# Performance work log

Measured on AMD Instinct MI355X. Metric: run time of the kernel, lower is better.

Reference implementation:

```python
import math
import jax, jax.numpy as jnp
import numpy as np
from jax import lax

N, C, H, W = 8, 256, 56, 56
S41, S42, S14 = 1, -1, 1  # fixed values for random roll shifts in original __init__


def setup_inputs() -> dict:
    key = jax.random.key(0)
    ks = jax.random.split(key, 9)
    c8 = C // 8
    x = jax.random.normal(ks[0], (N, C, H, W), jnp.float32)
    p2 = jax.random.normal(ks[1], (1, C, H, W), jnp.float32) * 0.02
    w6 = jax.random.normal(ks[2], (c8, C), jnp.float32) * (1.0 / math.sqrt(C))
    w7 = jax.random.normal(ks[3], (C, 9 * C), jnp.float32) * (1.0 / math.sqrt(9 * C))
    p9 = jax.random.normal(ks[4], (1, c8, H, W), jnp.float32) * 0.02
    b11 = math.sqrt(3.0 / c8)
    p11 = jax.random.uniform(ks[5], (c8, 1), jnp.float32, -b11, b11)
    w12 = jax.random.normal(ks[6], (C, 1, 3, 1), jnp.float32) * (1.0 / math.sqrt(3.0))
    w15 = jax.random.normal(ks[7], (C, C), jnp.float32) * (1.0 / math.sqrt(C))
    b16 = math.sqrt(3.0 / C)
    p16 = jax.random.uniform(ks[8], (C, H * W), jnp.float32, -b16, b16)
    return dict(x=x, p2=p2, w6=w6, w7=w7, p9=p9, p11=p11, w12=w12, w15=w15, p16=p16)


def _unfold33_d3(x):
    # F.unfold(x, (3,3), dilation=(3,3), padding=(3,3)) -> (n, c, 3, 3, h, w)
    xp = jnp.pad(x, ((0, 0), (0, 0), (3, 3), (3, 3)))
    rows = [jnp.stack([xp[:, :, 3 * i:3 * i + H, 3 * j:3 * j + W] for j in range(3)], axis=2)
            for i in range(3)]
    return jnp.stack(rows, axis=2)


def _forward(x, p2, w6, w7, p9, p11, w12, w15, p16):
    n = x.shape[0]
    s_hw = 1.0 / math.sqrt(H * W)
    s_c = 1.0 / math.sqrt(C)
    t1 = _unfold33_d3(x)                                    # n,c,3,3,h,w
    t2 = p2 * x
    t3 = t2 * t2
    t4 = jnp.roll(jnp.roll(t3, S41, axis=2), S42, axis=3)
    t5 = jax.nn.softmax(t4, axis=2)                          # softmax over h
    t6 = jnp.einsum('nchw,oc->nohw', t3, w6)                 # 1x1 conv c -> c//8
    t7 = jnp.einsum('nkhw,ok->nohw', t1.reshape(n, 9 * C, H, W), w7)  # 1x1 conv 9c -> c
    t8 = jnp.einsum('ncs,nds->ncd', t5.reshape(n, C, H * W), t3.reshape(n, C, H * W)) * s_hw
    t9 = p9 * t6
    t10 = jnp.maximum(t5, t7)
    t11 = jnp.einsum('nbhw,be->nehw', t9, p11)[:, 0]         # (n,h,w)
    # depthwise conv, kernel (3,1), dilation (2,1), padding (2,0)
    t12 = lax.conv_general_dilated(t10, w12, window_strides=(1, 1),
                                   padding=((2, 2), (0, 0)), rhs_dilation=(2, 1),
                                   feature_group_count=C,
                                   dimension_numbers=('NCHW', 'OIHW', 'NCHW'))
    t13 = t11[:, None] - t12                                 # (n,c,h,w)
    t14 = jnp.roll(x, S14, axis=2)
    t15 = jnp.einsum('nchw,oc->nohw', t14, w15)              # 1x1 conv c -> c
    t16 = jnp.einsum('nbc,bd->ndc', t8, p16)                 # (n, hw, c)
    t17 = t3 - t15
    t18 = t7 * t17
    t19 = jnp.einsum('ncs,nsd->ncd', t17.reshape(n, C, H * W), t16) * s_hw  # (n,c,c)
    t20 = (jnp.einsum('ndc,nds->ncs', t19, t13.reshape(n, C, H * W)) * s_c).reshape(n, C, H, W)
    return t20 + t18


def reference(x, p2, w6, w7, p9, p11, w12, w15, p16):
    return _forward(x, p2, w6, w7, p9, p11, w12, w15, p16)
```

## Files before the change

kernel.cpp:

```cpp
#include <hip/hip_runtime.h>

#define Nn 8
#define Cc 256
#define C8 32
#define Hh 56
#define Ww 56
#define HW 3136
#define CHW (Cc * HW)
#define K9C 2304
#define S_HW (1.0f / 56.0f)
#define S_C  0.0625f
#define XPLANE 3844
#define XPAD_ELEMS (Nn * XPLANE * Cc)

typedef float f4 __attribute__((ext_vector_type(4)));
typedef unsigned short ushort;
typedef __attribute__((ext_vector_type(4))) unsigned short u16x4;
typedef __attribute__((ext_vector_type(8))) unsigned short u16x8;
typedef __attribute__((ext_vector_type(8))) short short8;
typedef __attribute__((ext_vector_type(4))) float floatx4;

__device__ __forceinline__ ushort f2bf(float f) {
    union { float f; unsigned u; } v; v.f = f;
    unsigned r = v.u + 0x7FFF + ((v.u >> 16) & 1);
    return (ushort)(r >> 16);
}
__device__ __forceinline__ float bf2f(ushort u) {
    union { unsigned u; float f; } v; v.u = ((unsigned)u) << 16;
    return v.f;
}

__global__ __launch_bounds__(256) void k_t3(const float* __restrict__ x,
                                            const float* __restrict__ p2,
                                            float* __restrict__ t3,
                                            ushort* __restrict__ t3b) {
    int g = blockIdx.x * 256 + threadIdx.x;
    int idx = g * 4;
    int pidx = idx % CHW;
    f4 xv = *(const f4*)(x + idx);
    f4 pv = *(const f4*)(p2 + pidx);
    f4 t = xv * pv;
    f4 q = t * t;
    *(f4*)(t3 + idx) = q;
    u16x4 qb = { f2bf(q[0]), f2bf(q[1]), f2bf(q[2]), f2bf(q[3]) };
    *(u16x4*)(t3b + idx) = qb;
}

__global__ __launch_bounds__(256) void k_xT(const float* __restrict__ x,
                                            ushort* __restrict__ xpT) {
    __shared__ ushort Ts[112][40];
    int tid = threadIdx.x;
    int n = blockIdx.z;
    int c0 = blockIdx.y * 32;
    int s0 = blockIdx.x * 112;
    const float* xn = x + (size_t)n * CHW;
#pragma unroll
    for (int e = 0; e < 4; e++) {
        int lin = tid + e * 256;
        int sq = lin & 31;
        int c_l = lin >> 5;
        if (sq < 28) {
            f4 v = *(const f4*)(xn + (size_t)(c0 + c_l) * HW + s0 + sq * 4);
#pragma unroll
            for (int k = 0; k < 4; k++) Ts[sq * 4 + k][c_l] = f2bf(v[k]);
        }
    }
    __syncthreads();
    ushort* dstn = xpT + (size_t)n * (XPLANE * Cc);
#pragma unroll
    for (int e = 0; e < 2; e++) {
        int lin = tid + e * 256;
        int r = lin >> 2, ch = lin & 3;
        if (r < 112) {
            u16x8 v = *(const u16x8*)(&Ts[r][ch * 8]);
            int s_g = s0 + r;
            int h = s_g / 56;
            int wc = s_g - h * 56;
            size_t drow = (size_t)((h + 3) * 62 + wc + 3);
            *(u16x8*)(dstn + drow * Cc + c0 + ch * 8) = v;
        }
    }
}

__global__ __launch_bounds__(256) void k_w7p(const float* __restrict__ w7,
                                             ushort* __restrict__ w7p) {
    int g = blockIdx.x * 256 + threadIdx.x;
    int ij = g >> 16;
    int rem = g & 65535;
    int o = rem >> 8;
    int c = rem & 255;
    w7p[g] = f2bf(w7[(size_t)o * K9C + c * 9 + ij]);
}

__global__ __launch_bounds__(256) void k_cvt(const float* __restrict__ src,
                                             ushort* __restrict__ dst) {
    int g = blockIdx.x * 256 + threadIdx.x;
    dst[g] = f2bf(src[g]);
}

__global__ __launch_bounds__(256) void k_softmax(const float* __restrict__ t3,
                                                 ushort* __restrict__ t5b) {
    __shared__ float ld[HW];
    __shared__ float mx[Ww], rs[Ww];
    int tid = threadIdx.x;
    const float* src = t3 + (size_t)blockIdx.x * HW;
    for (int i = tid; i < HW; i += 256) ld[i] = src[i];
    __syncthreads();
    if (tid < Ww) {
        float m = -1e30f;
        for (int h = 0; h < Hh; h++) m = fmaxf(m, ld[h * Ww + tid]);
        float s = 0.f;
        for (int h = 0; h < Hh; h++) s += __expf(ld[h * Ww + tid] - m);
        mx[tid] = m;
        rs[tid] = 1.0f / s;
    }
    __syncthreads();
    ushort* dst = t5b + (size_t)blockIdx.x * HW;
    for (int i = tid; i < HW; i += 256) {
        int h = i / Ww, w = i - h * Ww;
        int wp = (w + 1 == Ww) ? 0 : w + 1;
        int hp = (h == 0) ? Hh - 1 : h - 1;
        dst[i] = f2bf(__expf(ld[hp * Ww + wp] - mx[wp]) * rs[wp]);
    }
}

__global__ __launch_bounds__(256, 3) void k_gemm_t7_mfma(
        const ushort* __restrict__ xpT,
        const ushort* __restrict__ w7p,
        float* __restrict__ t7) {
    __shared__ __align__(16) ushort Bs[620][40];
    int tid = threadIdx.x;
    int lane = tid & 63;
    int ln15 = lane & 15, quad = lane >> 4;
    int wave = tid >> 6;
    int wo = (wave >> 1) * 32;
    int wsx = (wave & 1) * 112;
    int n = blockIdx.z;
    int hb = blockIdx.y;
    int o0 = blockIdx.x * 64;
    const ushort* xT = xpT + (size_t)n * (XPLANE * Cc);
    size_t stageBase = (size_t)(hb * 248) * Cc;

    int sp0[7];
#pragma unroll
    for (int f = 0; f < 7; f++) {
        int s_l = wsx + f * 16 + ln15;
        int orow = s_l / 56;
        int wv = s_l - orow * 56;
        sp0[f] = orow * 62 + wv;
    }

    floatx4 acc[2][7] = {};

    for (int ct = 0; ct < Cc; ct += 32) {
        __syncthreads();
#pragma unroll
        for (int e = 0; e < 10; e++) {
            int lin = tid + e * 256;
            if (lin < 2480) {
                int sp = lin >> 2, ch = lin & 3;
                u16x8 v = *(const u16x8*)(xT + stageBase + (size_t)sp * Cc + ct + ch * 8);
                *(u16x8*)(&Bs[sp][ch * 8]) = v;
            }
        }
        __syncthreads();
        const ushort* wp = w7p + ct + quad * 8;
#pragma unroll
        for (int ij = 0; ij < 9; ij++) {
            int dsp = (ij / 3) * 186 + (ij % 3) * 3;
            short8 a0 = *(const short8*)(wp + (size_t)(ij * 256 + o0 + wo + ln15) * Cc);
            short8 a1 = *(const short8*)(wp + (size_t)(ij * 256 + o0 + wo + 16 + ln15) * Cc);
#pragma unroll
            for (int f = 0; f < 7; f++) {
                short8 b = *(const short8*)(&Bs[sp0[f] + dsp][quad * 8]);
                acc[0][f] = __builtin_amdgcn_mfma_f32_16x16x32_bf16(a0, b, acc[0][f], 0, 0, 0);
                acc[1][f] = __builtin_amdgcn_mfma_f32_16x16x32_bf16(a1, b, acc[1][f], 0, 0, 0);
            }
        }
    }

    float* t7n = t7 + (size_t)n * CHW;
    int sBase = hb * 224 + wsx;
#pragma unroll
    for (int m = 0; m < 2; m++) {
        int obase = o0 + wo + m * 16 + quad * 4;
#pragma unroll
        for (int f = 0; f < 7; f++) {
            int s = sBase + f * 16 + ln15;
#pragma unroll
            for (int r = 0; r < 4; r++)
                t7n[(size_t)(obase + r) * HW + s] = acc[m][f][r];
        }
    }
}

__global__ __launch_bounds__(256) void k_gemm_t15_mfma(const float* __restrict__ x,
                                                       const ushort* __restrict__ w15b,
                                                       const float* __restrict__ t3,
                                                       ushort* __restrict__ t17b) {
    __shared__ __align__(16) ushort As[128][40];
    __shared__ __align__(16) ushort Bs[128][40];
    int tid = threadIdx.x;
    int lane = tid & 63;
    int ln15 = lane & 15;
    int quad = lane >> 4;
    int wave = tid >> 6;
    int wm64 = (wave >> 1) * 64;
    int wn64 = (wave & 1) * 64;
    int n = blockIdx.z;
    int s0 = blockIdx.x * 128;
    int o0 = blockIdx.y * 128;
    const float* xn = x + (size_t)n * CHW;

    floatx4 acc[4][4] = {};

    for (int kt = 0; kt < Cc; kt += 32) {
#pragma unroll
        for (int e = 0; e < 2; e++) {
            int lin = tid + e * 256;
            int m = lin >> 2, kq = (lin & 3) * 8;
            *(u16x8*)(&As[m][kq]) =
                *(const u16x8*)(w15b + (size_t)(o0 + m) * Cc + kt + kq);
        }
#pragma unroll
        for (int e = 0; e < 4; e++) {
            int lin = tid + e * 256;
            int c_l = lin >> 5;
            int s4 = (lin & 31) * 4;
            int s = s0 + s4;
            int sc = s < HW ? s : HW - 4;
            int h = sc / Ww;
            int s_src = (h == 0) ? sc + 3080 : sc - 56;
            f4 v = *(const f4*)(xn + (size_t)(kt + c_l) * HW + s_src);
            Bs[s4 + 0][c_l] = f2bf(v[0]);
            Bs[s4 + 1][c_l] = f2bf(v[1]);
            Bs[s4 + 2][c_l] = f2bf(v[2]);
            Bs[s4 + 3][c_l] = f2bf(v[3]);
        }
        __syncthreads();

        short8 af[4], bf[4];
#pragma unroll
        for (int a = 0; a < 4; a++)
            af[a] = *(const short8*)(&As[wm64 + a * 16 + ln15][quad * 8]);
#pragma unroll
        for (int b = 0; b < 4; b++)
            bf[b] = *(const short8*)(&Bs[wn64 + b * 16 + ln15][quad * 8]);
#pragma unroll
        for (int a = 0; a < 4; a++)
#pragma unroll
            for (int b = 0; b < 4; b++)
                acc[a][b] = __builtin_amdgcn_mfma_f32_16x16x32_bf16(
                    af[a], bf[b], acc[a][b], 0, 0, 0);
        __syncthreads();
    }

    const float* t3n = t3 + (size_t)n * CHW;
    ushort* t17n = t17b + (size_t)n * CHW;
#pragma unroll
    for (int a = 0; a < 4; a++) {
        int obase = o0 + wm64 + a * 16 + quad * 4;
#pragma unroll
        for (int b = 0; b < 4; b++) {
            int s = s0 + wn64 + b * 16 + ln15;
            if (s < HW) {
#pragma unroll
                for (int r = 0; r < 4; r++) {
                    size_t idx = (size_t)(obase + r) * HW + s;
                    t17n[idx] = f2bf(t3n[idx] - acc[a][b][r]);
                }
            }
        }
    }
}

__global__ __launch_bounds__(256) void k_gemm_abt_mfma(const ushort* __restrict__ A,
                                                       const ushort* __restrict__ B,
                                                       long Bn,
                                                       float* __restrict__ outp,
                                                       float scale) {
    __shared__ __align__(16) ushort As[128][40];
    __shared__ __align__(16) ushort Bs[128][40];
    int tid = threadIdx.x;
    int lane = tid & 63;
    int ln15 = lane & 15;
    int quad = lane >> 4;
    int wave = tid >> 6;
    int wm64 = (wave >> 1) * 64;
    int wn64 = (wave & 1) * 64;
    int z = blockIdx.z;
    int n = z / 7, ks = z - n * 7;
    int d0 = blockIdx.x * 128;
    int c0 = blockIdx.y * 128;
    const ushort* An = A + (size_t)n * CHW;
    const ushort* Bb = B + (size_t)n * Bn;

    floatx4 acc[4][4] = {};
    int kbeg = ks * 448;

    for (int kt = kbeg; kt < kbeg + 448; kt += 32) {
#pragma unroll
        for (int e = 0; e < 2; e++) {
            int lin = tid + e * 256;
            int m = lin >> 2, kq = (lin & 3) * 8;
            *(u16x8*)(&As[m][kq]) =
                *(const u16x8*)(An + (size_t)(c0 + m) * HW + kt + kq);
            *(u16x8*)(&Bs[m][kq]) =
                *(const u16x8*)(Bb + (size_t)(d0 + m) * HW + kt + kq);
        }
        __syncthreads();

        short8 af[4], bf[4];
#pragma unroll
        for (int a = 0; a < 4; a++)
            af[a] = *(const short8*)(&As[wm64 + a * 16 + ln15][quad * 8]);
#pragma unroll
        for (int b = 0; b < 4; b++)
            bf[b] = *(const short8*)(&Bs[wn64 + b * 16 + ln15][quad * 8]);
#pragma unroll
        for (int a = 0; a < 4; a++)
#pragma unroll
            for (int b = 0; b < 4; b++)
                acc[a][b] = __builtin_amdgcn_mfma_f32_16x16x32_bf16(
                    af[a], bf[b], acc[a][b], 0, 0, 0);
        __syncthreads();
    }

    float* on = outp + (size_t)n * (Cc * Cc);
#pragma unroll
    for (int a = 0; a < 4; a++) {
        int cbase = c0 + wm64 + a * 16 + quad * 4;
#pragma unroll
        for (int b = 0; b < 4; b++) {
            int d = d0 + wn64 + b * 16 + ln15;
#pragma unroll
            for (int r = 0; r < 4; r++)
                atomicAdd(&on[(size_t)(cbase + r) * Cc + d], acc[a][b][r] * scale);
        }
    }
}

__global__ __launch_bounds__(256) void k_gemm_t19(const float* __restrict__ u,
                                                  const float* __restrict__ t8,
                                                  ushort* __restrict__ t19Tb) {
    __shared__ float As[64][20];
    __shared__ float Bs[16][68];
    int tid = threadIdx.x;
    int tx = tid & 15, ty = tid >> 4;
    int n = blockIdx.z;
    int d0 = blockIdx.x * 64;
    int c0 = blockIdx.y * 64;
    const float* un = u + (size_t)n * Cc * Cc;
    const float* t8n = t8 + (size_t)n * Cc * Cc;
    f4 acc[4] = {};
    for (int kt = 0; kt < Cc; kt += 16) {
        int lin = tid * 4;
        {
            int r = lin >> 4, kq = lin & 15;
            *(f4*)(&As[r][kq]) = *(const f4*)(un + (size_t)(c0 + r) * Cc + kt + kq);
        }
        {
            int kk = lin >> 6, col = lin & 63;
            *(f4*)(&Bs[kk][col]) = *(const f4*)(t8n + (size_t)(kt + kk) * Cc + d0 + col);
        }
        __syncthreads();
#pragma unroll
        for (int kk = 0; kk < 16; kk += 4) {
            f4 av[4], bv[4];
#pragma unroll
            for (int a = 0; a < 4; a++) av[a] = *(const f4*)(&As[ty * 4 + a][kk]);
#pragma unroll
            for (int q = 0; q < 4; q++) bv[q] = *(const f4*)(&Bs[kk + q][tx * 4]);
#pragma unroll
            for (int a = 0; a < 4; a++)
#pragma unroll
                for (int q = 0; q < 4; q++) acc[a] += av[a][q] * bv[q];
        }
        __syncthreads();
    }
    ushort* on = t19Tb + (size_t)n * Cc * Cc;
#pragma unroll
    for (int a = 0; a < 4; a++) {
        int c = c0 + ty * 4 + a;
#pragma unroll
        for (int j = 0; j < 4; j++)
            on[(size_t)(d0 + tx * 4 + j) * Cc + c] = f2bf(acc[a][j] * S_HW);
    }
}

__global__ __launch_bounds__(256) void k_t11(const float* __restrict__ t3,
                                             const float* __restrict__ w6,
                                             const float* __restrict__ p9,
                                             const float* __restrict__ p11,
                                             float* __restrict__ t11) {
    __shared__ float smem[8704];
    float* w6s = smem;
    float* part = smem;
    float* part2 = smem + 8448;
    int tid = threadIdx.x;
    for (int i = tid; i < C8 * Cc; i += 256) w6s[i] = w6[i];
    __syncthreads();
    int n = blockIdx.y;
    int sl = tid & 63;
    int cg = tid >> 6;
    int s = blockIdx.x * 64 + sl;
    const float* t3n = t3 + (size_t)n * CHW + s;
    float acc[C8] = {};
    for (int c = cg * 64; c < cg * 64 + 64; c += 4) {
        float v0 = t3n[(c + 0) * HW];
        float v1 = t3n[(c + 1) * HW];
        float v2 = t3n[(c + 2) * HW];
        float v3 = t3n[(c + 3) * HW];
#pragma unroll
        for (int b = 0; b < C8; b++) {
            f4 wv = *(const f4*)(&w6s[b * Cc + c]);
            acc[b] += wv[0] * v0 + wv[1] * v1 + wv[2] * v2 + wv[3] * v3;
        }
    }
    __syncthreads();
#pragma unroll
    for (int b = 0; b < C8; b++) part[(cg * 64 + sl) * 33 + b] = acc[b];
    __syncthreads();
    float r = 0.f;
#pragma unroll
    for (int j = 0; j < 8; j++) {
        int b = cg * 8 + j;
        float sum = part[(0 * 64 + sl) * 33 + b] + part[(1 * 64 + sl) * 33 + b] +
                    part[(2 * 64 + sl) * 33 + b] + part[(3 * 64 + sl) * 33 + b];
        r += p11[b] * p9[b * HW + s] * sum;
    }
    part2[cg * 64 + sl] = r;
    __syncthreads();
    if (tid < 64)
        t11[(size_t)n * HW + s] = part2[sl] + part2[64 + sl] + part2[128 + sl] + part2[192 + sl];
}

__global__ __launch_bounds__(256) void k_t13(const ushort* __restrict__ t5b,
                                             const float* __restrict__ t7,
                                             const float* __restrict__ t11,
                                             const float* __restrict__ w12,
                                             ushort* __restrict__ t13b) {
    int g = blockIdx.x * 256 + threadIdx.x;
    int s = g % HW;
    int nc = g / HW;
    int c = nc % Cc;
    int n = nc / Cc;
    int h = s / Ww, w = s - h * Ww;
    float sum = 0.f;
#pragma unroll
    for (int kh = 0; kh < 3; kh++) {
        int hh = h - 2 + 2 * kh;
        if ((unsigned)hh < (unsigned)Hh) {
            size_t idx = (size_t)nc * HW + hh * Ww + w;
            float t10 = fmaxf(bf2f(t5b[idx]), t7[idx]);
            sum += w12[c * 3 + kh] * t10;
        }
    }
    t13b[g] = f2bf(t11[(size_t)n * HW + s] - sum);
}

__global__ __launch_bounds__(256) void k_gemm_out_mfma(const ushort* __restrict__ t19Tb,
                                                       const ushort* __restrict__ t13b,
                                                       const float* __restrict__ t7,
                                                       const ushort* __restrict__ t17b,
                                                       float* __restrict__ outp) {
    __shared__ __align__(16) ushort As[128][40];
    __shared__ __align__(16) ushort Bs[128][40];
    int tid = threadIdx.x;
    int lane = tid & 63;
    int ln15 = lane & 15;
    int quad = lane >> 4;
    int wave = tid >> 6;
    int wm64 = (wave >> 1) * 64;
    int wn64 = (wave & 1) * 64;
    int n = blockIdx.z;
    int s0 = blockIdx.x * 128;
    int c0 = blockIdx.y * 128;
    const ushort* An = t19Tb + (size_t)n * Cc * Cc;
    const ushort* t13n = t13b + (size_t)n * CHW;

    floatx4 acc[4][4] = {};

    for (int kt = 0; kt < Cc; kt += 32) {
#pragma unroll
        for (int e = 0; e < 2; e++) {
            int lin = tid + e * 256;
            int m = lin >> 2, kq = (lin & 3) * 8;
            *(u16x8*)(&As[m][kq]) =
                *(const u16x8*)(An + (size_t)(c0 + m) * Cc + kt + kq);
        }
#pragma unroll
        for (int e = 0; e < 2; e++) {
            int lin = tid + e * 256;
            int d_l = lin >> 4;
            int s8 = (lin & 15) * 8;
            int s = s0 + s8;
            int sc = s <= HW - 8 ? s : HW - 8;
            u16x8 v = *(const u16x8*)(t13n + (size_t)(kt + d_l) * HW + sc);
#pragma unroll
            for (int j = 0; j < 8; j++) Bs[s8 + j][d_l] = v[j];
        }
        __syncthreads();

        short8 af[4], bf[4];
#pragma unroll
        for (int a = 0; a < 4; a++)
            af[a] = *(const short8*)(&As[wm64 + a * 16 + ln15][quad * 8]);
#pragma unroll
        for (int b = 0; b < 4; b++)
            bf[b] = *(const short8*)(&Bs[wn64 + b * 16 + ln15][quad * 8]);
#pragma unroll
        for (int a = 0; a < 4; a++)
#pragma unroll
            for (int b = 0; b < 4; b++)
                acc[a][b] = __builtin_amdgcn_mfma_f32_16x16x32_bf16(
                    af[a], bf[b], acc[a][b], 0, 0, 0);
        __syncthreads();
    }

    const float* t7n = t7 + (size_t)n * CHW;
    const ushort* t17n = t17b + (size_t)n * CHW;
    float* on = outp + (size_t)n * CHW;
#pragma unroll
    for (int a = 0; a < 4; a++) {
        int cbase = c0 + wm64 + a * 16 + quad * 4;
#pragma unroll
        for (int b = 0; b < 4; b++) {
            int s = s0 + wn64 + b * 16 + ln15;
            if (s < HW) {
#pragma unroll
                for (int r = 0; r < 4; r++) {
                    size_t idx = (size_t)(cbase + r) * HW + s;
                    on[idx] = acc[a][b][r] * S_C + t7n[idx] * bf2f(t17n[idx]);
                }
            }
        }
    }
}

extern "C" void kernel_launch(void* const* d_in, const int* in_sizes, int n_in,
                              void* d_out, int out_size, void* d_ws, size_t ws_size,
                              hipStream_t stream) {
    const float* x   = (const float*)d_in[0];
    const float* p2  = (const float*)d_in[1];
    const float* w6  = (const float*)d_in[2];
    const float* w7  = (const float*)d_in[3];
    const float* p9  = (const float*)d_in[4];
    const float* p11 = (const float*)d_in[5];
    const float* w12 = (const float*)d_in[6];
    const float* w15 = (const float*)d_in[7];
    const float* p16 = (const float*)d_in[8];
    float* ws = (float*)d_ws;

    float* t3  = ws;
    float* t7  = ws + 6422528;
    float* t8  = ws + 12845056;
    float* uu  = ws + 13369344;
    float* t11 = ws + 13893632;
    ushort* ub  = (ushort*)(ws + 13919232);
    ushort* t5b   = ub;
    ushort* t3b   = ub + 6422528;
    ushort* t17b  = ub + 12845056;
    ushort* t13b  = ub + 19267584;
    ushort* xpT   = ub + 25690112;
    ushort* w7p   = ub + 33562624;
    ushort* w15b  = ub + 34152448;
    ushort* p16b  = ub + 34217984;
    ushort* t19Tb = ub + 35020800;
    float* outp = (float*)d_out;

    hipMemsetAsync(xpT, 0, (size_t)XPAD_ELEMS * 2, stream);
    k_t3<<<dim3(6272), dim3(256), 0, stream>>>(x, p2, t3, t3b);
    k_xT<<<dim3(28, 8, Nn), dim3(256), 0, stream>>>(x, xpT);
    k_w7p<<<dim3(2304), dim3(256), 0, stream>>>(w7, w7p);
    k_cvt<<<dim3(256),  dim3(256), 0, stream>>>(w15, w15b);
    k_cvt<<<dim3(3136), dim3(256), 0, stream>>>(p16, p16b);
    k_softmax<<<dim3(Nn * Cc), dim3(256), 0, stream>>>(t3, t5b);
    hipMemsetAsync(t8, 0, (size_t)Nn * Cc * Cc * 4, stream);
    hipMemsetAsync(uu, 0, (size_t)Nn * Cc * Cc * 4, stream);
    k_gemm_t7_mfma<<<dim3(4, 14, Nn), dim3(256), 0, stream>>>(xpT, w7p, t7);
    k_gemm_t15_mfma<<<dim3(25, 2, Nn), dim3(256), 0, stream>>>(x, w15b, t3, t17b);
    k_gemm_abt_mfma<<<dim3(2, 2, Nn * 7), dim3(256), 0, stream>>>(t5b, t3b, (long)CHW, t8, S_HW);
    k_t11<<<dim3(49, 8), dim3(256), 0, stream>>>(t3, w6, p9, p11, t11);
    k_gemm_abt_mfma<<<dim3(2, 2, Nn * 7), dim3(256), 0, stream>>>(t17b, p16b, 0L, uu, 1.0f);
    k_gemm_t19<<<dim3(4, 4, Nn), dim3(256), 0, stream>>>(uu, t8, t19Tb);
    k_t13<<<dim3(25088), dim3(256), 0, stream>>>(t5b, t7, t11, w12, t13b);
    k_gemm_out_mfma<<<dim3(25, 2, Nn), dim3(256), 0, stream>>>(t19Tb, t13b, t7, t17b, outp);
}
```

Baseline: 361.6 us.

## Fuse t3 with softmax, store intermediates in bf16, merge abt GEMMs, prefetch t7 stage

Merges the t3 elementwise kernel with the softmax so t3 is produced in shared memory and never written in fp32. t7 is stored as bf16, and t15 reads the pre-transposed padded bf16 x buffer instead of transposing fp32 x itself. The two split-K ABᵀ GEMMs become one launch, the t7 GEMM prefetches its next stage into registers, and t13 is vectorised to four elements per thread. The aim is less HBM traffic and fewer launches, at the cost of extra bf16 rounding on t3 and t7 in later stages and higher register pressure in the t7 GEMM.

```diff
diff --git a/kernel.cpp b/kernel.cpp
--- a/kernel.cpp
+++ b/kernel.cpp
@@ -30,20 +30,44 @@
     return v.f;
 }
 
-__global__ __launch_bounds__(256) void k_t3(const float* __restrict__ x,
-                                            const float* __restrict__ p2,
-                                            float* __restrict__ t3,
-                                            ushort* __restrict__ t3b) {
-    int g = blockIdx.x * 256 + threadIdx.x;
-    int idx = g * 4;
-    int pidx = idx % CHW;
-    f4 xv = *(const f4*)(x + idx);
-    f4 pv = *(const f4*)(p2 + pidx);
-    f4 t = xv * pv;
-    f4 q = t * t;
-    *(f4*)(t3 + idx) = q;
-    u16x4 qb = { f2bf(q[0]), f2bf(q[1]), f2bf(q[2]), f2bf(q[3]) };
-    *(u16x4*)(t3b + idx) = qb;
+__global__ __launch_bounds__(256) void k_t3sm(const float* __restrict__ x,
+                                              const float* __restrict__ p2,
+                                              ushort* __restrict__ t3b,
+                                              ushort* __restrict__ t5b) {
+    __shared__ float ld[HW];
+    __shared__ float mx[Ww], rs[Ww];
+    int tid = threadIdx.x;
+    int nc = blockIdx.x;
+    int c = nc & 255;
+    const float* xn = x + (size_t)nc * HW;
+    const float* pp = p2 + (size_t)c * HW;
+    ushort* t3n = t3b + (size_t)nc * HW;
+    for (int i = tid; i < 784; i += 256) {
+        f4 xv = *(const f4*)(xn + i * 4);
+        f4 pv = *(const f4*)(pp + i * 4);
+        f4 t = xv * pv;
+        f4 q = t * t;
+        *(f4*)(&ld[i * 4]) = q;
+        u16x4 qb = { f2bf(q[0]), f2bf(q[1]), f2bf(q[2]), f2bf(q[3]) };
+        *(u16x4*)(t3n + i * 4) = qb;
+    }
+    __syncthreads();
+    if (tid < Ww) {
+        float m = -1e30f;
+        for (int h = 0; h < Hh; h++) m = fmaxf(m, ld[h * Ww + tid]);
+        float s = 0.f;
+        for (int h = 0; h < Hh; h++) s += __expf(ld[h * Ww + tid] - m);
+        mx[tid] = m;
+        rs[tid] = 1.0f / s;
+    }
+    __syncthreads();
+    ushort* dst = t5b + (size_t)nc * HW;
+    for (int i = tid; i < HW; i += 256) {
+        int h = i / Ww, w = i - h * Ww;
+        int wp = (w + 1 == Ww) ? 0 : w + 1;
+        int hp = (h == 0) ? Hh - 1 : h - 1;
+        dst[i] = f2bf(__expf(ld[hp * Ww + wp] - mx[wp]) * rs[wp]);
+    }
 }
 
 __global__ __launch_bounds__(256) void k_xT(const float* __restrict__ x,
@@ -98,36 +122,10 @@
     dst[g] = f2bf(src[g]);
 }
 
-__global__ __launch_bounds__(256) void k_softmax(const float* __restrict__ t3,
-                                                 ushort* __restrict__ t5b) {
-    __shared__ float ld[HW];
-    __shared__ float mx[Ww], rs[Ww];
-    int tid = threadIdx.x;
-    const float* src = t3 + (size_t)blockIdx.x * HW;
-    for (int i = tid; i < HW; i += 256) ld[i] = src[i];
-    __syncthreads();
-    if (tid < Ww) {
-        float m = -1e30f;
-        for (int h = 0; h < Hh; h++) m = fmaxf(m, ld[h * Ww + tid]);
-        float s = 0.f;
-        for (int h = 0; h < Hh; h++) s += __expf(ld[h * Ww + tid] - m);
-        mx[tid] = m;
-        rs[tid] = 1.0f / s;
-    }
-    __syncthreads();
-    ushort* dst = t5b + (size_t)blockIdx.x * HW;
-    for (int i = tid; i < HW; i += 256) {
-        int h = i / Ww, w = i - h * Ww;
-        int wp = (w + 1 == Ww) ? 0 : w + 1;
-        int hp = (h == 0) ? Hh - 1 : h - 1;
-        dst[i] = f2bf(__expf(ld[hp * Ww + wp] - mx[wp]) * rs[wp]);
-    }
-}
-
 __global__ __launch_bounds__(256, 3) void k_gemm_t7_mfma(
         const ushort* __restrict__ xpT,
         const ushort* __restrict__ w7p,
-        float* __restrict__ t7) {
+        ushort* __restrict__ t7b) {
     __shared__ __align__(16) ushort Bs[620][40];
     int tid = threadIdx.x;
     int lane = tid & 63;
@@ -138,8 +136,7 @@
     int n = blockIdx.z;
     int hb = blockIdx.y;
     int o0 = blockIdx.x * 64;
-    const ushort* xT = xpT + (size_t)n * (XPLANE * Cc);
-    size_t stageBase = (size_t)(hb * 248) * Cc;
+    const ushort* stagePtr = xpT + (size_t)n * (XPLANE * Cc) + (size_t)(hb * 248) * Cc;
 
     int sp0[7];
 #pragma unroll
@@ -151,19 +148,31 @@
     }
 
     floatx4 acc[2][7] = {};
+    u16x8 pre[10];
+#pragma unroll
+    for (int e = 0; e < 10; e++) {
+        int lin = tid + e * 256;
+        if (lin < 2480)
+            pre[e] = *(const u16x8*)(stagePtr + (size_t)(lin >> 2) * Cc + (lin & 3) * 8);
+    }
 
     for (int ct = 0; ct < Cc; ct += 32) {
-        __syncthreads();
 #pragma unroll
         for (int e = 0; e < 10; e++) {
             int lin = tid + e * 256;
-            if (lin < 2480) {
-                int sp = lin >> 2, ch = lin & 3;
-                u16x8 v = *(const u16x8*)(xT + stageBase + (size_t)sp * Cc + ct + ch * 8);
-                *(u16x8*)(&Bs[sp][ch * 8]) = v;
+            if (lin < 2480)
+                *(u16x8*)(&Bs[lin >> 2][(lin & 3) * 8]) = pre[e];
+        }
+        __syncthreads();
+        if (ct + 32 < Cc) {
+#pragma unroll
+            for (int e = 0; e < 10; e++) {
+                int lin = tid + e * 256;
+                if (lin < 2480)
+                    pre[e] = *(const u16x8*)(stagePtr + (size_t)(lin >> 2) * Cc +
+                                             ct + 32 + (lin & 3) * 8);
             }
         }
-        __syncthreads();
         const ushort* wp = w7p + ct + quad * 8;
 #pragma unroll
         for (int ij = 0; ij < 9; ij++) {
@@ -177,9 +186,10 @@
                 acc[1][f] = __builtin_amdgcn_mfma_f32_16x16x32_bf16(a1, b, acc[1][f], 0, 0, 0);
             }
         }
-    }
-
-    float* t7n = t7 + (size_t)n * CHW;
+        __syncthreads();
+    }
+
+    ushort* t7n = t7b + (size_t)n * CHW;
     int sBase = hb * 224 + wsx;
 #pragma unroll
     for (int m = 0; m < 2; m++) {
@@ -189,14 +199,14 @@
             int s = sBase + f * 16 + ln15;
 #pragma unroll
             for (int r = 0; r < 4; r++)
-                t7n[(size_t)(obase + r) * HW + s] = acc[m][f][r];
-        }
-    }
-}
-
-__global__ __launch_bounds__(256) void k_gemm_t15_mfma(const float* __restrict__ x,
+                t7n[(size_t)(obase + r) * HW + s] = f2bf(acc[m][f][r]);
+        }
+    }
+}
+
+__global__ __launch_bounds__(256) void k_gemm_t15_mfma(const ushort* __restrict__ xpT,
                                                        const ushort* __restrict__ w15b,
-                                                       const float* __restrict__ t3,
+                                                       const ushort* __restrict__ t3b,
                                                        ushort* __restrict__ t17b) {
     __shared__ __align__(16) ushort As[128][40];
     __shared__ __align__(16) ushort Bs[128][40];
@@ -210,7 +220,19 @@
     int n = blockIdx.z;
     int s0 = blockIdx.x * 128;
     int o0 = blockIdx.y * 128;
-    const float* xn = x + (size_t)n * CHW;
+    const ushort* xT = xpT + (size_t)n * (XPLANE * Cc);
+
+    int sp_src[2];
+#pragma unroll
+    for (int e = 0; e < 2; e++) {
+        int s_l = (tid + e * 256) >> 2;
+        int s = s0 + s_l;
+        int sc = s < HW ? s : HW - 1;
+        int h = sc / Ww, w = sc - h * Ww;
+        int hp = (h == 0) ? 58 : h + 2;
+        sp_src[e] = hp * 62 + w + 3;
+    }
+    int chq = (tid & 3) * 8;
 
     floatx4 acc[4][4] = {};
 
@@ -223,19 +245,10 @@
                 *(const u16x8*)(w15b + (size_t)(o0 + m) * Cc + kt + kq);
         }
 #pragma unroll
-        for (int e = 0; e < 4; e++) {
-            int lin = tid + e * 256;
-            int c_l = lin >> 5;
-            int s4 = (lin & 31) * 4;
-            int s = s0 + s4;
-            int sc = s < HW ? s : HW - 4;
-            int h = sc / Ww;
-            int s_src = (h == 0) ? sc + 3080 : sc - 56;
-            f4 v = *(const f4*)(xn + (size_t)(kt + c_l) * HW + s_src);
-            Bs[s4 + 0][c_l] = f2bf(v[0]);
-            Bs[s4 + 1][c_l] = f2bf(v[1]);
-            Bs[s4 + 2][c_l] = f2bf(v[2]);
-            Bs[s4 + 3][c_l] = f2bf(v[3]);
+        for (int e = 0; e < 2; e++) {
+            int s_l = (tid + e * 256) >> 2;
+            *(u16x8*)(&Bs[s_l][chq]) =
+                *(const u16x8*)(xT + (size_t)sp_src[e] * Cc + kt + chq);
         }
         __syncthreads();
 
@@ -255,7 +268,7 @@
         __syncthreads();
     }
 
-    const float* t3n = t3 + (size_t)n * CHW;
+    const ushort* t3n = t3b + (size_t)n * CHW;
     ushort* t17n = t17b + (size_t)n * CHW;
 #pragma unroll
     for (int a = 0; a < 4; a++) {
@@ -267,18 +280,19 @@
 #pragma unroll
                 for (int r = 0; r < 4; r++) {
                     size_t idx = (size_t)(obase + r) * HW + s;
-                    t17n[idx] = f2bf(t3n[idx] - acc[a][b][r]);
+                    t17n[idx] = f2bf(bf2f(t3n[idx]) - acc[a][b][r]);
                 }
             }
         }
     }
 }
 
-__global__ __launch_bounds__(256) void k_gemm_abt_mfma(const ushort* __restrict__ A,
-                                                       const ushort* __restrict__ B,
-                                                       long Bn,
-                                                       float* __restrict__ outp,
-                                                       float scale) {
+__global__ __launch_bounds__(256) void k_abt2(const ushort* __restrict__ t5b,
+                                              const ushort* __restrict__ t3b,
+                                              const ushort* __restrict__ t17b,
+                                              const ushort* __restrict__ p16b,
+                                              float* __restrict__ t8,
+                                              float* __restrict__ uu) {
     __shared__ __align__(16) ushort As[128][40];
     __shared__ __align__(16) ushort Bs[128][40];
     int tid = threadIdx.x;
@@ -288,12 +302,15 @@
     int wave = tid >> 6;
     int wm64 = (wave >> 1) * 64;
     int wn64 = (wave & 1) * 64;
+    int sel = blockIdx.y >> 1;
+    int c0 = (blockIdx.y & 1) * 128;
+    int d0 = blockIdx.x * 128;
     int z = blockIdx.z;
     int n = z / 7, ks = z - n * 7;
-    int d0 = blockIdx.x * 128;
-    int c0 = blockIdx.y * 128;
-    const ushort* An = A + (size_t)n * CHW;
-    const ushort* Bb = B + (size_t)n * Bn;
+    const ushort* An = (sel ? t17b : t5b) + (size_t)n * CHW;
+    const ushort* Bb = sel ? p16b : (t3b + (size_t)n * CHW);
+    float* outp = (sel ? uu : t8) + (size_t)n * (Cc * Cc);
+    float scale = sel ? 1.0f : S_HW;
 
     floatx4 acc[4][4] = {};
     int kbeg = ks * 448;
@@ -326,7 +343,6 @@
         __syncthreads();
     }
 
-    float* on = outp + (size_t)n * (Cc * Cc);
 #pragma unroll
     for (int a = 0; a < 4; a++) {
         int cbase = c0 + wm64 + a * 16 + quad * 4;
@@ -335,7 +351,7 @@
             int d = d0 + wn64 + b * 16 + ln15;
 #pragma unroll
             for (int r = 0; r < 4; r++)
-                atomicAdd(&on[(size_t)(cbase + r) * Cc + d], acc[a][b][r] * scale);
+                atomicAdd(&outp[(size_t)(cbase + r) * Cc + d], acc[a][b][r] * scale);
         }
     }
 }
@@ -388,7 +404,7 @@
     }
 }
 
-__global__ __launch_bounds__(256) void k_t11(const float* __restrict__ t3,
+__global__ __launch_bounds__(256) void k_t11(const ushort* __restrict__ t3b,
                                              const float* __restrict__ w6,
                                              const float* __restrict__ p9,
                                              const float* __restrict__ p11,
@@ -404,13 +420,13 @@
     int sl = tid & 63;
     int cg = tid >> 6;
     int s = blockIdx.x * 64 + sl;
-    const float* t3n = t3 + (size_t)n * CHW + s;
+    const ushort* t3n = t3b + (size_t)n * CHW + s;
     float acc[C8] = {};
     for (int c = cg * 64; c < cg * 64 + 64; c += 4) {
-        float v0 = t3n[(c + 0) * HW];
-        float v1 = t3n[(c + 1) * HW];
-        float v2 = t3n[(c + 2) * HW];
-        float v3 = t3n[(c + 3) * HW];
+        float v0 = bf2f(t3n[(c + 0) * HW]);
+        float v1 = bf2f(t3n[(c + 1) * HW]);
+        float v2 = bf2f(t3n[(c + 2) * HW]);
+        float v3 = bf2f(t3n[(c + 3) * HW]);
 #pragma unroll
         for (int b = 0; b < C8; b++) {
             f4 wv = *(const f4*)(&w6s[b * Cc + c]);
@@ -436,32 +452,40 @@
 }
 
 __global__ __launch_bounds__(256) void k_t13(const ushort* __restrict__ t5b,
-                                             const float* __restrict__ t7,
+                                             const ushort* __restrict__ t7b,
                                              const float* __restrict__ t11,
                                              const float* __restrict__ w12,
                                              ushort* __restrict__ t13b) {
     int g = blockIdx.x * 256 + threadIdx.x;
-    int s = g % HW;
-    int nc = g / HW;
-    int c = nc % Cc;
-    int n = nc / Cc;
+    int idx = g * 4;
+    int nc = idx / HW;
+    int s = idx - nc * HW;
+    int c = nc & 255;
+    int n = nc >> 8;
     int h = s / Ww, w = s - h * Ww;
-    float sum = 0.f;
+    f4 sum = {0.f, 0.f, 0.f, 0.f};
 #pragma unroll
     for (int kh = 0; kh < 3; kh++) {
         int hh = h - 2 + 2 * kh;
         if ((unsigned)hh < (unsigned)Hh) {
-            size_t idx = (size_t)nc * HW + hh * Ww + w;
-            float t10 = fmaxf(bf2f(t5b[idx]), t7[idx]);
-            sum += w12[c * 3 + kh] * t10;
-        }
-    }
-    t13b[g] = f2bf(t11[(size_t)n * HW + s] - sum);
+            size_t base = (size_t)nc * HW + hh * Ww + w;
+            u16x4 t5v = *(const u16x4*)(t5b + base);
+            u16x4 t7v = *(const u16x4*)(t7b + base);
+            float wk = w12[c * 3 + kh];
+#pragma unroll
+            for (int j = 0; j < 4; j++)
+                sum[j] += wk * fmaxf(bf2f(t5v[j]), bf2f(t7v[j]));
+        }
+    }
+    f4 t11v = *(const f4*)(t11 + (size_t)n * HW + s);
+    u16x4 o = { f2bf(t11v[0] - sum[0]), f2bf(t11v[1] - sum[1]),
+                f2bf(t11v[2] - sum[2]), f2bf(t11v[3] - sum[3]) };
+    *(u16x4*)(t13b + idx) = o;
 }
 
 __global__ __launch_bounds__(256) void k_gemm_out_mfma(const ushort* __restrict__ t19Tb,
                                                        const ushort* __restrict__ t13b,
-                                                       const float* __restrict__ t7,
+                                                       const ushort* __restrict__ t7b,
                                                        const ushort* __restrict__ t17b,
                                                        float* __restrict__ outp) {
     __shared__ __align__(16) ushort As[128][40];
@@ -518,7 +542,7 @@
         __syncthreads();
     }
 
-    const float* t7n = t7 + (size_t)n * CHW;
+    const ushort* t7n = t7b + (size_t)n * CHW;
     const ushort* t17n = t17b + (size_t)n * CHW;
     float* on = outp + (size_t)n * CHW;
 #pragma unroll
@@ -531,7 +555,7 @@
 #pragma unroll
                 for (int r = 0; r < 4; r++) {
                     size_t idx = (size_t)(cbase + r) * HW + s;
-                    on[idx] = acc[a][b][r] * S_C + t7n[idx] * bf2f(t17n[idx]);
+                    on[idx] = acc[a][b][r] * S_C + bf2f(t7n[idx]) * bf2f(t17n[idx]);
                 }
             }
         }
@@ -552,38 +576,35 @@
     const float* p16 = (const float*)d_in[8];
     float* ws = (float*)d_ws;
 
-    float* t3  = ws;
-    float* t7  = ws + 6422528;
-    float* t8  = ws + 12845056;
-    float* uu  = ws + 13369344;
-    float* t11 = ws + 13893632;
-    ushort* ub  = (ushort*)(ws + 13919232);
+    float* t8  = ws;
+    float* uu  = ws + 524288;
+    float* t11 = ws + 1048576;
+    ushort* ub  = (ushort*)(ws + 1081344);
     ushort* t5b   = ub;
     ushort* t3b   = ub + 6422528;
     ushort* t17b  = ub + 12845056;
     ushort* t13b  = ub + 19267584;
-    ushort* xpT   = ub + 25690112;
-    ushort* w7p   = ub + 33562624;
-    ushort* w15b  = ub + 34152448;
-    ushort* p16b  = ub + 34217984;
-    ushort* t19Tb = ub + 35020800;
+    ushort* t7b   = ub + 25690112;
+    ushort* xpT   = ub + 32112640;
+    ushort* w7p   = ub + 39985152;
+    ushort* w15b  = ub + 40574976;
+    ushort* p16b  = ub + 40640512;
+    ushort* t19Tb = ub + 41443328;
     float* outp = (float*)d_out;
 
     hipMemsetAsync(xpT, 0, (size_t)XPAD_ELEMS * 2, stream);
-    k_t3<<<dim3(6272), dim3(256), 0, stream>>>(x, p2, t3, t3b);
+    k_t3sm<<<dim3(Nn * Cc), dim3(256), 0, stream>>>(x, p2, t3b, t5b);
     k_xT<<<dim3(28, 8, Nn), dim3(256), 0, stream>>>(x, xpT);
     k_w7p<<<dim3(2304), dim3(256), 0, stream>>>(w7, w7p);
     k_cvt<<<dim3(256),  dim3(256), 0, stream>>>(w15, w15b);
     k_cvt<<<dim3(3136), dim3(256), 0, stream>>>(p16, p16b);
-    k_softmax<<<dim3(Nn * Cc), dim3(256), 0, stream>>>(t3, t5b);
     hipMemsetAsync(t8, 0, (size_t)Nn * Cc * Cc * 4, stream);
     hipMemsetAsync(uu, 0, (size_t)Nn * Cc * Cc * 4, stream);
-    k_gemm_t7_mfma<<<dim3(4, 14, Nn), dim3(256), 0, stream>>>(xpT, w7p, t7);
-    k_gemm_t15_mfma<<<dim3(25, 2, Nn), dim3(256), 0, stream>>>(x, w15b, t3, t17b);
-    k_gemm_abt_mfma<<<dim3(2, 2, Nn * 7), dim3(256), 0, stream>>>(t5b, t3b, (long)CHW, t8, S_HW);
-    k_t11<<<dim3(49, 8), dim3(256), 0, stream>>>(t3, w6, p9, p11, t11);
-    k_gemm_abt_mfma<<<dim3(2, 2, Nn * 7), dim3(256), 0, stream>>>(t17b, p16b, 0L, uu, 1.0f);
+    k_gemm_t7_mfma<<<dim3(4, 14, Nn), dim3(256), 0, stream>>>(xpT, w7p, t7b);
+    k_gemm_t15_mfma<<<dim3(25, 2, Nn), dim3(256), 0, stream>>>(xpT, w15b, t3b, t17b);
+    k_abt2<<<dim3(2, 4, Nn * 7), dim3(256), 0, stream>>>(t5b, t3b, t17b, p16b, t8, uu);
+    k_t11<<<dim3(49, Nn), dim3(256), 0, stream>>>(t3b, w6, p9, p11, t11);
     k_gemm_t19<<<dim3(4, 4, Nn), dim3(256), 0, stream>>>(uu, t8, t19Tb);
-    k_t13<<<dim3(25088), dim3(256), 0, stream>>>(t5b, t7, t11, w12, t13b);
-    k_gemm_out_mfma<<<dim3(25, 2, Nn), dim3(256), 0, stream>>>(t19Tb, t13b, t7, t17b, outp);
-}
+    k_t13<<<dim3(6272), dim3(256), 0, stream>>>(t5b, t7b, t11, w12, t13b);
+    k_gemm_out_mfma<<<dim3(25, 2, Nn), dim3(256), 0, stream>>>(t19Tb, t13b, t7b, t17b, outp);
+}
```

Result: no change. 361.6 us (+0.0%).
